# Kernel optimization log

Measured on AMD Instinct MI355X. Metric: run time of the kernel, lower is better.

Reference implementation:

```python
import jax, jax.numpy as jnp
import numpy as np

B, CIN, COUT = 16, 32, 64
H = W = 64
K = 3                      # kernel side
GRID_SIZE, SPLINE_ORDER = 5, 3
P = K * K                  # in_features of each KANLinear
GR0, GR1 = -1.0, 1.0       # grid_range


def make_grid():
    # torch: grid = arange(-k, G+k+1)*h + grid_range[0], expanded to (in_features, G+2k+1)
    h = (GR1 - GR0) / GRID_SIZE
    g = jnp.arange(-SPLINE_ORDER, GRID_SIZE + SPLINE_ORDER + 1, dtype=jnp.float32) * h + GR0
    return jnp.broadcast_to(g, (P, g.shape[0]))


def b_splines(x, grid):
    # Cox-de Boor recursion. x: (..., P) -> bases: (..., P, GRID_SIZE+SPLINE_ORDER)
    xe = x[..., None]
    bases = ((xe >= grid[:, :-1]) & (xe < grid[:, 1:])).astype(x.dtype)
    for j in range(1, SPLINE_ORDER + 1):
        left = (xe - grid[:, : -(j + 1)]) / (grid[:, j:-1] - grid[:, : -(j + 1)])
        right = (grid[:, j + 1 :] - xe) / (grid[:, j + 1 :] - grid[:, 1:-j])
        bases = left * bases[..., :-1] + right * bases[..., 1:]
    return bases


def setup_inputs() -> dict:
    key = jax.random.key(0)
    k1, k2, k3, k4 = jax.random.split(key, 4)
    x = jax.random.normal(k1, (B, CIN, H, W), dtype=jnp.float32)
    base_weight = jax.random.normal(k2, (COUT, CIN, P), dtype=jnp.float32) * (1.0 / np.sqrt(P))
    spline_weight = jax.random.normal(k3, (COUT, CIN, P, GRID_SIZE + SPLINE_ORDER), dtype=jnp.float32) * 0.1
    spline_scaler = jax.random.normal(k4, (COUT, CIN, P), dtype=jnp.float32) * (1.0 / np.sqrt(P))
    return {"x": x, "base_weight": base_weight, "spline_weight": spline_weight, "spline_scaler": spline_scaler}


def reference(x, base_weight, spline_weight, spline_scaler):
    grid = make_grid()
    # im2col like torch.nn.Unfold: (B, CIN*P, Hout, Wout), channel-major feature order
    patches = jax.lax.conv_general_dilated_patches(x, (K, K), (1, 1), "VALID")
    _, _, Ho, Wo = patches.shape
    patches = patches.reshape(B, CIN, P, Ho * Wo).transpose(0, 1, 3, 2)  # (B, CIN, L, P)
    # base branch: SiLU(x) @ base_weight^T, summed over input channels per output channel
    base_out = jnp.einsum("bclp,ocp->bol", jax.nn.silu(patches), base_weight)
    # spline branch: B-spline bases contracted with scaled spline weights
    bases = b_splines(patches, grid)                       # (B, CIN, L, P, G+k)
    scaled_w = spline_weight * spline_scaler[..., None]    # (COUT, CIN, P, G+k)
    spline_out = jnp.einsum("bclpg,ocpg->bol", bases, scaled_w)
    return (base_out + spline_out).reshape(B, COUT, Ho, Wo)
```

## Files before the change

kernel.cpp:

```cpp
#include <hip/hip_runtime.h>


typedef short v8s __attribute__((ext_vector_type(8)));
typedef float v4f __attribute__((ext_vector_type(4)));

#define FSPL8_OFF   0u
#define FSILU_OFF   16777472u
#define WPACK8_OFF  20972032u
#define WPACKS_OFF  21119744u

__device__ __forceinline__ unsigned short f2bf(float f) {
  unsigned int u = __float_as_uint(f);
  u += 0x7fffu + ((u >> 16) & 1u);
  return (unsigned short)(u >> 16);
}

__global__ __launch_bounds__(256) void k_spline(const float* __restrict__ x,
                                                unsigned char* __restrict__ ws) {
  int pix = blockIdx.x * 256 + threadIdx.x;
  float v = x[pix];
  float bb[11];
#pragma unroll
  for (int i = 0; i < 11; ++i) {
    float t0 = -2.2f + 0.4f * i;
    bb[i] = (v >= t0 && v < t0 + 0.4f) ? 1.0f : 0.0f;
  }
#pragma unroll
  for (int j = 1; j <= 3; ++j) {
    float rj = 1.0f / (0.4f * j);
#pragma unroll
    for (int i = 0; i + j < 11; ++i) {
      float ti = -2.2f + 0.4f * i;
      float lf = (v - ti) * rj;
      float rt = ((ti + 0.4f * (j + 1)) - v) * rj;
      bb[i] = lf * bb[i] + rt * bb[i + 1];
    }
  }
  uint2 o;
  unsigned w0 = __builtin_amdgcn_cvt_pk_fp8_f32(bb[0], bb[1], 0, false);
  w0 = __builtin_amdgcn_cvt_pk_fp8_f32(bb[2], bb[3], w0, true);
  unsigned w1 = __builtin_amdgcn_cvt_pk_fp8_f32(bb[4], bb[5], 0, false);
  w1 = __builtin_amdgcn_cvt_pk_fp8_f32(bb[6], bb[7], w1, true);
  o.x = w0; o.y = w1;
  *(uint2*)(ws + FSPL8_OFF + (size_t)pix * 8) = o;
}

__global__ __launch_bounds__(256) void k_silu(const float* __restrict__ x,
                                              unsigned char* __restrict__ ws) {
  int bid = blockIdx.x;
  int b = bid >> 6, y = bid & 63;
  int t = threadIdx.x;
  int xx = t & 63, cg = t >> 6;
  unsigned short h[8];
#pragma unroll
  for (int k = 0; k < 8; ++k) {
    int c = cg * 8 + k;
    float v = x[(((size_t)(b * 32 + c) * 64 + y) * 64) + xx];
    float s = v / (1.0f + __expf(-v));
    h[k] = f2bf(s);
  }
  uint4 o;
  o.x = (unsigned)h[0] | ((unsigned)h[1] << 16);
  o.y = (unsigned)h[2] | ((unsigned)h[3] << 16);
  o.z = (unsigned)h[4] | ((unsigned)h[5] << 16);
  o.w = (unsigned)h[6] | ((unsigned)h[7] << 16);
  *(uint4*)(ws + FSILU_OFF + (size_t)(b * 4096 + y * 64 + xx) * 64 + cg * 16) = o;
}

__global__ __launch_bounds__(256) void k_wpack(const float* __restrict__ bw,
                                               const float* __restrict__ sw,
                                               const float* __restrict__ sc,
                                               unsigned char* __restrict__ ws) {
  int tid = blockIdx.x * 256 + threadIdx.x;
  if (tid >= 165888) return;
  if (tid < 147456) {
    int e = tid & 7, lane = (tid >> 3) & 63, ot = (tid >> 9) & 3, s = tid >> 11;
    int k = s * 32 + ((lane >> 4) << 3) + e;
    int o = (ot << 4) + (lane & 15);
    int chunk = k / 24, u = k - chunk * 24;
    int dj = u >> 3, g = u & 7;
    int c = chunk / 3, di = chunk - c * 3;
    int p = di * 3 + dj;
    float val = sw[((size_t)(o * 32 + c) * 9 + p) * 8 + g] * sc[(size_t)(o * 32 + c) * 9 + p];
    ws[WPACK8_OFF + tid] =
        (unsigned char)(__builtin_amdgcn_cvt_pk_fp8_f32(val, 0.f, 0, false) & 0xff);
  } else {
    int t2 = tid - 147456;
    int e = t2 & 7, lane = (t2 >> 3) & 63, ot = (t2 >> 9) & 3, sp = t2 >> 11;
    int o = (ot << 4) + (lane & 15);
    int cc = ((lane >> 4) << 3) + e;
    float val = bw[(size_t)(o * 32 + cc) * 9 + sp];
    *(unsigned short*)(ws + WPACKS_OFF + (size_t)t2 * 2) = f2bf(val);
  }
}

__device__ __forceinline__ void ld16(unsigned char* ldsp, const unsigned char* gp) {
  __builtin_amdgcn_global_load_lds(
      (const __attribute__((address_space(1))) unsigned int*)gp,
      (__attribute__((address_space(3))) unsigned int*)ldsp, 16, 0, 0);
}

__global__ __launch_bounds__(512) void k_gemm(const unsigned char* __restrict__ ws,
                                              float* __restrict__ out) {
  __shared__ __align__(16) unsigned char wl8[2][18432];
  __shared__ __align__(16) unsigned char fl8[2][12544];
  __shared__ __align__(16) unsigned char wsil[36864];
  __shared__ __align__(16) unsigned char fsil[25088];

  const int blk = blockIdx.x;
  const int b = blk >> 4, ig = blk & 15;
  const int i0 = ig * 4;
  const int tid = threadIdx.x;
  const int wave = tid >> 6, lane = tid & 63;
  const int q = lane >> 4, ln = lane & 15;
  const int r = wave >> 1, oh = wave & 1;
  const int i = i0 + r;

  auto stage_spl = [&](int t, int bi) {
#pragma unroll
    for (int it = 0; it < 4; ++it) {
      const int u = wave + it * 8;
      if (u < 18) {
        ld16(&wl8[bi][u * 1024],
             ws + WPACK8_OFF + (size_t)t * 18432 + (size_t)u * 1024 + lane * 16);
      } else if (u < 30) {
        const int v = u - 18;
        const int cp = v / 3, cr = v - cp * 3;
        ld16(&fl8[bi][v * 1024],
             ws + FSPL8_OFF +
                 ((size_t)((b * 32 + t * 4 + cp) * 64 + i0 + cr * 2)) * 512 + lane * 16);
      }
    }
  };

  auto stage_silu = [&]() {
#pragma unroll
    for (int it = 0; it < 8; ++it) {
      const int u = wave + it * 8;
      if (u < 36) {
        ld16(&wsil[u * 1024], ws + WPACKS_OFF + (size_t)u * 1024 + lane * 16);
      } else if (u < 60) {
        const int v = u - 36;
        const int rr = v >> 2, p4 = v & 3;
        const int y = min(i0 + rr, 63);
        ld16(&fsil[v * 1024],
             ws + FSILU_OFF + (size_t)(b * 64 + y) * 4096 +
                 (p4 * 16 + (lane >> 2)) * 64 + ((lane & 3) ^ ((lane >> 2) & 3)) * 16);
      }
    }
  };

  int foff[9];
#pragma unroll
  for (int sg = 0; sg < 9; ++sg) {
    int rid = 4 * sg + q;
    int ch = rid / 3, sub = rid - ch * 3;
    int cp = ch / 3, di = ch - cp * 3;
    foff[sg] = cp * 3072 + (r + di) * 512 + (sub + ln) * 8;
  }

  v4f acc[2][4];
#pragma unroll
  for (int a = 0; a < 2; ++a)
#pragma unroll
    for (int c = 0; c < 4; ++c) acc[a][c] = (v4f){0.f, 0.f, 0.f, 0.f};

  stage_silu();
  stage_spl(0, 0);
  __syncthreads();

#pragma unroll 1
  for (int t = 0; t < 8; ++t) {
    if (t < 7) stage_spl(t + 1, (t + 1) & 1);
    const unsigned char* wb_base = wl8[t & 1];
    const unsigned char* fb_base = fl8[t & 1];
#pragma unroll
    for (int sg = 0; sg < 9; ++sg) {
      long wb[2], fb[4];
#pragma unroll
      for (int tt = 0; tt < 2; ++tt)
        wb[tt] = *(const long*)(wb_base + sg * 2048 + (oh * 2 + tt) * 512 + lane * 8);
#pragma unroll
      for (int pt = 0; pt < 4; ++pt)
        fb[pt] = *(const long*)(fb_base + foff[sg] + pt * 128);
#pragma unroll
      for (int tt = 0; tt < 2; ++tt)
#pragma unroll
        for (int pt = 0; pt < 4; ++pt)
          acc[tt][pt] = __builtin_amdgcn_mfma_f32_16x16x32_fp8_fp8(
              wb[tt], fb[pt], acc[tt][pt], 0, 0, 0);
    }
    __syncthreads();
  }

#pragma unroll
  for (int e = 0; e < 9; ++e) {
    const int di = e / 3, dj = e % 3;
    v8s wb[2], fb[4];
#pragma unroll
    for (int tt = 0; tt < 2; ++tt)
      wb[tt] = *(const v8s*)(&wsil[0] + e * 4096 + (oh * 2 + tt) * 1024 + lane * 16);
    const int xb = dj + ln;
    const int sbase = (r + di) * 4096 + xb * 64 + ((q ^ (xb & 3)) * 16);
#pragma unroll
    for (int pt = 0; pt < 4; ++pt)
      fb[pt] = *(const v8s*)(&fsil[0] + sbase + pt * 1024);
#pragma unroll
    for (int tt = 0; tt < 2; ++tt)
#pragma unroll
      for (int pt = 0; pt < 4; ++pt)
        acc[tt][pt] = __builtin_amdgcn_mfma_f32_16x16x32_bf16(
            wb[tt], fb[pt], acc[tt][pt], 0, 0, 0);
  }

  if (i < 62) {
#pragma unroll
    for (int tt = 0; tt < 2; ++tt)
#pragma unroll
      for (int pt = 0; pt < 4; ++pt) {
        const int j = pt * 16 + ln;
        if (j < 62) {
#pragma unroll
          for (int rr = 0; rr < 4; ++rr) {
            const int o = (oh * 2 + tt) * 16 + q * 4 + rr;
            out[(((size_t)b * 64 + o) * 62 + i) * 62 + j] = acc[tt][pt][rr];
          }
        }
      }
  }
}

extern "C" void kernel_launch(void* const* d_in, const int* in_sizes, int n_in,
                              void* d_out, int out_size, void* d_ws, size_t ws_size,
                              hipStream_t stream) {
  const float* x  = (const float*)d_in[0];
  const float* bw = (const float*)d_in[1];
  const float* sw = (const float*)d_in[2];
  const float* sc = (const float*)d_in[3];
  unsigned char* ws = (unsigned char*)d_ws;
  float* out = (float*)d_out;

  hipLaunchKernelGGL(k_spline, dim3(8192), dim3(256), 0, stream, x, ws);
  hipLaunchKernelGGL(k_silu,   dim3(1024), dim3(256), 0, stream, x, ws);
  hipLaunchKernelGGL(k_wpack,  dim3(648),  dim3(256), 0, stream, bw, sw, sc, ws);
  hipLaunchKernelGGL(k_gemm,   dim3(256),  dim3(512), 0, stream, ws, out);
}
```

Before: 103.6 us.

## Fuse spline and SiLU feature kernels and use 16x16x128 scaled FP8 MFMA

Merges the spline-basis and SiLU preprocessing kernels into one that reads x once and writes both feature buffers, saving a launch and a second pass over the input. Inside the GEMM, the spline contraction is re-tiled so 256 of each 288-wide K chunk runs on the MI355X 16x16x128 f8f6f4 scaled MFMA with unit scales, and the remaining 32 run on the older 16x16x32 FP8 MFMA. The weight-packing kernel gains a matching layout split into an MX region and a tail FP8 region. This cuts the MFMA instruction count but makes feature gathering more complex, with four 8-byte LDS loads per operand, and the fused feature kernel now does more work per thread.

```diff
diff --git a/kernel.cpp b/kernel.cpp
--- a/kernel.cpp
+++ b/kernel.cpp
@@ -3,11 +3,16 @@
 
 typedef short v8s __attribute__((ext_vector_type(8)));
 typedef float v4f __attribute__((ext_vector_type(4)));
+typedef int   v4i __attribute__((ext_vector_type(4)));
+typedef int   v8i __attribute__((ext_vector_type(8)));
 
 #define FSPL8_OFF   0u
 #define FSILU_OFF   16777472u
-#define WPACK8_OFF  20972032u
-#define WPACKS_OFF  21119744u
+#define WMX_OFF     20972032u
+#define WF8_OFF     21103104u
+#define WPACKS_OFF  21119488u
+
+#define SCALE1 0x7F7F7F7Fu
 
 __device__ __forceinline__ unsigned short f2bf(float f) {
   unsigned int u = __float_as_uint(f);
@@ -15,56 +20,47 @@
   return (unsigned short)(u >> 16);
 }
 
-__global__ __launch_bounds__(256) void k_spline(const float* __restrict__ x,
-                                                unsigned char* __restrict__ ws) {
-  int pix = blockIdx.x * 256 + threadIdx.x;
-  float v = x[pix];
-  float bb[11];
-#pragma unroll
-  for (int i = 0; i < 11; ++i) {
-    float t0 = -2.2f + 0.4f * i;
-    bb[i] = (v >= t0 && v < t0 + 0.4f) ? 1.0f : 0.0f;
-  }
-#pragma unroll
-  for (int j = 1; j <= 3; ++j) {
-    float rj = 1.0f / (0.4f * j);
-#pragma unroll
-    for (int i = 0; i + j < 11; ++i) {
-      float ti = -2.2f + 0.4f * i;
-      float lf = (v - ti) * rj;
-      float rt = ((ti + 0.4f * (j + 1)) - v) * rj;
-      bb[i] = lf * bb[i] + rt * bb[i + 1];
-    }
-  }
-  uint2 o;
-  unsigned w0 = __builtin_amdgcn_cvt_pk_fp8_f32(bb[0], bb[1], 0, false);
-  w0 = __builtin_amdgcn_cvt_pk_fp8_f32(bb[2], bb[3], w0, true);
-  unsigned w1 = __builtin_amdgcn_cvt_pk_fp8_f32(bb[4], bb[5], 0, false);
-  w1 = __builtin_amdgcn_cvt_pk_fp8_f32(bb[6], bb[7], w1, true);
-  o.x = w0; o.y = w1;
-  *(uint2*)(ws + FSPL8_OFF + (size_t)pix * 8) = o;
-}
-
-__global__ __launch_bounds__(256) void k_silu(const float* __restrict__ x,
+__global__ __launch_bounds__(256) void k_feat(const float* __restrict__ x,
                                               unsigned char* __restrict__ ws) {
-  int bid = blockIdx.x;
-  int b = bid >> 6, y = bid & 63;
-  int t = threadIdx.x;
-  int xx = t & 63, cg = t >> 6;
+  const int bid = blockIdx.x;
+  const int b = bid >> 6, y = bid & 63;
+  const int t = threadIdx.x;
+  const int xx = t & 63, cg = t >> 6;
   unsigned short h[8];
 #pragma unroll
   for (int k = 0; k < 8; ++k) {
-    int c = cg * 8 + k;
-    float v = x[(((size_t)(b * 32 + c) * 64 + y) * 64) + xx];
-    float s = v / (1.0f + __expf(-v));
-    h[k] = f2bf(s);
-  }
-  uint4 o;
-  o.x = (unsigned)h[0] | ((unsigned)h[1] << 16);
-  o.y = (unsigned)h[2] | ((unsigned)h[3] << 16);
-  o.z = (unsigned)h[4] | ((unsigned)h[5] << 16);
-  o.w = (unsigned)h[6] | ((unsigned)h[7] << 16);
-  *(uint4*)(ws + FSILU_OFF + (size_t)(b * 4096 + y * 64 + xx) * 64 + cg * 16) = o;
+    const int c = cg * 8 + k;
+    const float v = x[(((size_t)(b * 32 + c) * 64 + y) * 64) + xx];
+    h[k] = f2bf(v / (1.0f + __expf(-v)));
+    float bb[11];
+#pragma unroll
+    for (int i = 0; i < 11; ++i) {
+      float t0 = -2.2f + 0.4f * i;
+      bb[i] = (v >= t0 && v < t0 + 0.4f) ? 1.0f : 0.0f;
+    }
+#pragma unroll
+    for (int j = 1; j <= 3; ++j) {
+      float rj = 1.0f / (0.4f * j);
+#pragma unroll
+      for (int i = 0; i + j < 11; ++i) {
+        float ti = -2.2f + 0.4f * i;
+        bb[i] = (v - ti) * rj * bb[i] + ((ti + 0.4f * (j + 1)) - v) * rj * bb[i + 1];
+      }
+    }
+    uint2 o;
+    unsigned w0 = __builtin_amdgcn_cvt_pk_fp8_f32(bb[0], bb[1], 0, false);
+    w0 = __builtin_amdgcn_cvt_pk_fp8_f32(bb[2], bb[3], w0, true);
+    unsigned w1 = __builtin_amdgcn_cvt_pk_fp8_f32(bb[4], bb[5], 0, false);
+    w1 = __builtin_amdgcn_cvt_pk_fp8_f32(bb[6], bb[7], w1, true);
+    o.x = w0; o.y = w1;
+    *(uint2*)(ws + FSPL8_OFF + ((((size_t)(b * 32 + c) * 64 + y) * 64) + xx) * 8) = o;
+  }
+  uint4 s;
+  s.x = (unsigned)h[0] | ((unsigned)h[1] << 16);
+  s.y = (unsigned)h[2] | ((unsigned)h[3] << 16);
+  s.z = (unsigned)h[4] | ((unsigned)h[5] << 16);
+  s.w = (unsigned)h[6] | ((unsigned)h[7] << 16);
+  *(uint4*)(ws + FSILU_OFF + (size_t)(b * 4096 + y * 64 + xx) * 64 + cg * 16) = s;
 }
 
 __global__ __launch_bounds__(256) void k_wpack(const float* __restrict__ bw,
@@ -74,16 +70,28 @@
   int tid = blockIdx.x * 256 + threadIdx.x;
   if (tid >= 165888) return;
   if (tid < 147456) {
-    int e = tid & 7, lane = (tid >> 3) & 63, ot = (tid >> 9) & 3, s = tid >> 11;
-    int k = s * 32 + ((lane >> 4) << 3) + e;
+    int k, dst;
+    if (tid < 131072) {
+      int bh = tid & 15, lane = (tid >> 4) & 63, pc = (tid >> 10) & 1;
+      int ss = (tid >> 13) & 1, p = tid >> 14;
+      k = p * 288 + ss * 128 + (lane >> 4) * 32 + pc * 16 + bh;
+      dst = WMX_OFF + tid;
+    } else {
+      int t2 = tid - 131072;
+      int e = t2 & 7, lane = (t2 >> 3) & 63, p = t2 >> 11;
+      k = p * 288 + 256 + (lane >> 4) * 8 + e;
+      dst = WF8_OFF + t2;
+    }
+    int ot = (tid < 131072) ? ((tid >> 11) & 3) : (((tid - 131072) >> 9) & 3);
+    int lane = (tid < 131072) ? ((tid >> 4) & 63) : (((tid - 131072) >> 3) & 63);
     int o = (ot << 4) + (lane & 15);
     int chunk = k / 24, u = k - chunk * 24;
     int dj = u >> 3, g = u & 7;
     int c = chunk / 3, di = chunk - c * 3;
-    int p = di * 3 + dj;
-    float val = sw[((size_t)(o * 32 + c) * 9 + p) * 8 + g] * sc[(size_t)(o * 32 + c) * 9 + p];
-    ws[WPACK8_OFF + tid] =
-        (unsigned char)(__builtin_amdgcn_cvt_pk_fp8_f32(val, 0.f, 0, false) & 0xff);
+    int p_tap = di * 3 + dj;
+    float val = sw[((size_t)(o * 32 + c) * 9 + p_tap) * 8 + g] *
+                sc[(size_t)(o * 32 + c) * 9 + p_tap];
+    ws[dst] = (unsigned char)(__builtin_amdgcn_cvt_pk_fp8_f32(val, 0.f, 0, false) & 0xff);
   } else {
     int t2 = tid - 147456;
     int e = t2 & 7, lane = (t2 >> 3) & 63, ot = (t2 >> 9) & 3, sp = t2 >> 11;
@@ -116,19 +124,19 @@
   const int r = wave >> 1, oh = wave & 1;
   const int i = i0 + r;
 
-  auto stage_spl = [&](int t, int bi) {
+  auto stage_spl = [&](int p, int bi) {
 #pragma unroll
     for (int it = 0; it < 4; ++it) {
       const int u = wave + it * 8;
-      if (u < 18) {
-        ld16(&wl8[bi][u * 1024],
-             ws + WPACK8_OFF + (size_t)t * 18432 + (size_t)u * 1024 + lane * 16);
+      if (u < 16) {
+        ld16(&wl8[bi][u * 1024], ws + WMX_OFF + (size_t)p * 16384 + (size_t)u * 1024 + lane * 16);
+      } else if (u < 18) {
+        ld16(&wl8[bi][u * 1024], ws + WF8_OFF + (size_t)p * 2048 + (size_t)(u - 16) * 1024 + lane * 16);
       } else if (u < 30) {
         const int v = u - 18;
         const int cp = v / 3, cr = v - cp * 3;
         ld16(&fl8[bi][v * 1024],
-             ws + FSPL8_OFF +
-                 ((size_t)((b * 32 + t * 4 + cp) * 64 + i0 + cr * 2)) * 512 + lane * 16);
+             ws + FSPL8_OFF + ((size_t)((b * 32 + p * 4 + cp) * 64 + i0 + cr * 2)) * 512 + lane * 16);
       }
     }
   };
@@ -150,14 +158,16 @@
     }
   };
 
-  int foff[9];
-#pragma unroll
-  for (int sg = 0; sg < 9; ++sg) {
-    int rid = 4 * sg + q;
+  auto offf = [&](int sg, int qq) {
+    int rid = 4 * sg + qq;
     int ch = rid / 3, sub = rid - ch * 3;
     int cp = ch / 3, di = ch - cp * 3;
-    foff[sg] = cp * 3072 + (r + di) * 512 + (sub + ln) * 8;
-  }
+    return cp * 3072 + (r + di) * 512 + (sub + ln) * 8;
+  };
+  int offA[4], offB[4];
+#pragma unroll
+  for (int qq = 0; qq < 4; ++qq) { offA[qq] = offf(q, qq); offB[qq] = offf(4 + q, qq); }
+  const int off8 = offf(8, q);
 
   v4f acc[2][4];
 #pragma unroll
@@ -172,23 +182,45 @@
 #pragma unroll 1
   for (int t = 0; t < 8; ++t) {
     if (t < 7) stage_spl(t + 1, (t + 1) & 1);
-    const unsigned char* wb_base = wl8[t & 1];
-    const unsigned char* fb_base = fl8[t & 1];
-#pragma unroll
-    for (int sg = 0; sg < 9; ++sg) {
-      long wb[2], fb[4];
+    const unsigned char* wb = wl8[t & 1];
+    const unsigned char* fb = fl8[t & 1];
+#pragma unroll
+    for (int ss = 0; ss < 2; ++ss) {
+      union { v8i v; v4i h[2]; } wf[2];
+#pragma unroll
+      for (int tt = 0; tt < 2; ++tt) {
+        const unsigned char* wp = wb + ss * 8192 + (oh * 2 + tt) * 2048 + lane * 16;
+        wf[tt].h[0] = *(const v4i*)(wp);
+        wf[tt].h[1] = *(const v4i*)(wp + 1024);
+      }
+      const int* offs = ss ? offB : offA;
+      union { v8i v; long l[4]; } ff[4];
+#pragma unroll
+      for (int pt = 0; pt < 4; ++pt)
+#pragma unroll
+        for (int qq = 0; qq < 4; ++qq)
+          ff[pt].l[qq] = *(const long*)(fb + offs[qq] + pt * 128);
 #pragma unroll
       for (int tt = 0; tt < 2; ++tt)
-        wb[tt] = *(const long*)(wb_base + sg * 2048 + (oh * 2 + tt) * 512 + lane * 8);
+#pragma unroll
+        for (int pt = 0; pt < 4; ++pt)
+          acc[tt][pt] = __builtin_amdgcn_mfma_scale_f32_16x16x128_f8f6f4(
+              wf[tt].v, ff[pt].v, acc[tt][pt], 0, 0, 0, SCALE1, 0, SCALE1);
+    }
+    {
+      long w8[2], f8[4];
+#pragma unroll
+      for (int tt = 0; tt < 2; ++tt)
+        w8[tt] = *(const long*)(wb + 16384 + (oh * 2 + tt) * 512 + lane * 8);
 #pragma unroll
       for (int pt = 0; pt < 4; ++pt)
-        fb[pt] = *(const long*)(fb_base + foff[sg] + pt * 128);
+        f8[pt] = *(const long*)(fb + off8 + pt * 128);
 #pragma unroll
       for (int tt = 0; tt < 2; ++tt)
 #pragma unroll
         for (int pt = 0; pt < 4; ++pt)
           acc[tt][pt] = __builtin_amdgcn_mfma_f32_16x16x32_fp8_fp8(
-              wb[tt], fb[pt], acc[tt][pt], 0, 0, 0);
+              w8[tt], f8[pt], acc[tt][pt], 0, 0, 0);
     }
     __syncthreads();
   }
@@ -196,21 +228,21 @@
 #pragma unroll
   for (int e = 0; e < 9; ++e) {
     const int di = e / 3, dj = e % 3;
-    v8s wb[2], fb[4];
+    v8s wb2[2], fb2[4];
 #pragma unroll
     for (int tt = 0; tt < 2; ++tt)
-      wb[tt] = *(const v8s*)(&wsil[0] + e * 4096 + (oh * 2 + tt) * 1024 + lane * 16);
+      wb2[tt] = *(const v8s*)(&wsil[0] + e * 4096 + (oh * 2 + tt) * 1024 + lane * 16);
     const int xb = dj + ln;
     const int sbase = (r + di) * 4096 + xb * 64 + ((q ^ (xb & 3)) * 16);
 #pragma unroll
     for (int pt = 0; pt < 4; ++pt)
-      fb[pt] = *(const v8s*)(&fsil[0] + sbase + pt * 1024);
+      fb2[pt] = *(const v8s*)(&fsil[0] + sbase + pt * 1024);
 #pragma unroll
     for (int tt = 0; tt < 2; ++tt)
 #pragma unroll
       for (int pt = 0; pt < 4; ++pt)
         acc[tt][pt] = __builtin_amdgcn_mfma_f32_16x16x32_bf16(
-            wb[tt], fb[pt], acc[tt][pt], 0, 0, 0);
+            wb2[tt], fb2[pt], acc[tt][pt], 0, 0, 0);
   }
 
   if (i < 62) {
@@ -240,8 +272,7 @@
   unsigned char* ws = (unsigned char*)d_ws;
   float* out = (float*)d_out;
 
-  hipLaunchKernelGGL(k_spline, dim3(8192), dim3(256), 0, stream, x, ws);
-  hipLaunchKernelGGL(k_silu,   dim3(1024), dim3(256), 0, stream, x, ws);
-  hipLaunchKernelGGL(k_wpack,  dim3(648),  dim3(256), 0, stream, bw, sw, sc, ws);
-  hipLaunchKernelGGL(k_gemm,   dim3(256),  dim3(512), 0, stream, ws, out);
-}
+  hipLaunchKernelGGL(k_feat,  dim3(1024), dim3(256), 0, stream, x, ws);
+  hipLaunchKernelGGL(k_wpack, dim3(648),  dim3(256), 0, stream, bw, sw, sc, ws);
+  hipLaunchKernelGGL(k_gemm,  dim3(256),  dim3(512), 0, stream, ws, out);
+}
```

After: 100.2 us. 1.03x faster.
